# Kernel optimization log

Measured on AMD Instinct MI355X. Metric: run time of the kernel, lower is better.

Reference implementation:

```python
import jax, jax.numpy as jnp
import numpy as np

KS = 2
K = 3 * KS**2 + 3 * KS + 1  # 19 hex-stencil sites
MUL = 16                     # multiplicity of each irrep block
C0 = 0.28209479177387814     # Y_0 integral-normalized, 1/(2*sqrt(pi))
C1 = 0.4886025119029199      # Y_1 coeff, sqrt(3/(4*pi))


def _hex_offsets(ks):
    """Hexagonal stencil offsets in the exact order of spin2coltri2d (center first)."""
    hexagon = [[1, 1], [1, 0], [0, -1], [-1, -1], [-1, 0], [0, 1]]
    offs = [(0, 0)]
    for k in range(1, ks + 1):
        for l in range(6 * k):
            eb = hexagon[l // k]
            ea = hexagon[(l // k + 1) % 6]
            offs.append((eb[0] * (k - l % k) + ea[0] * (l % k),
                         eb[1] * (k - l % k) + ea[1] * (l % k)))
    return offs  # length K


def setup_inputs() -> dict:
    key = jax.random.key(0)
    k1, k2, k3, k4, k5, k6, k7 = jax.random.split(key, 7)
    N, Lx, Ly = 4, 128, 128
    feat = jax.random.normal(k1, (N, Lx, Ly, 4 * MUL), dtype=jnp.float32)
    spin = jax.random.normal(k2, (N, Lx, Ly, 3), dtype=jnp.float32)
    # 'uvw' TensorProduct weights: one (mul_in, mul_out) block per hex position per path
    wshape = (K, MUL, MUL)
    w000 = jax.random.normal(k3, wshape, dtype=jnp.float32)  # 0e x 0e -> 0e
    w011 = jax.random.normal(k4, wshape, dtype=jnp.float32)  # 0e x 1e -> 1e
    w101 = jax.random.normal(k5, wshape, dtype=jnp.float32)  # 1e x 0e -> 1e
    w110 = jax.random.normal(k6, wshape, dtype=jnp.float32)  # 1e x 1e -> 0e (dot)
    w111 = jax.random.normal(k7, wshape, dtype=jnp.float32)  # 1e x 1e -> 1e (cross)
    return {"feat": feat, "spin": spin, "w000": w000, "w011": w011,
            "w101": w101, "w110": w110, "w111": w111}


def reference(feat, spin, w000, w011, w101, w110, w111):
    # --- spin2coltri2d: circular hex-stencil gather via rolls (no pad copy) ---
    offs = _hex_offsets(KS)
    col = jnp.stack([jnp.roll(feat, shift=(-ox, -oy), axis=(1, 2))
                     for (ox, oy) in offs], axis=3)  # (N,Lx,Ly,K,64)
    s = col[..., :MUL]                                       # scalars (N,Lx,Ly,K,16)
    v = col[..., MUL:].reshape(col.shape[:4] + (MUL, 3))     # vectors (N,Lx,Ly,K,16,3)
    # --- spherical harmonics of spin, l=0..1, normalize=False, integral norm ---
    sh1 = C1 * spin[..., jnp.array([1, 2, 0])]               # e3nn l=1 order (y,z,x)
    # --- CG tensor product, path-normalized per output irrep ---
    a_s = 1.0 / np.sqrt(2 * K * MUL)   # two paths feed scalar out
    a_v = 1.0 / np.sqrt(3 * K * MUL)   # three paths feed vector out
    out_s = C0 * jnp.einsum('nxyku,kuw->nxyw', s, w000)
    out_s = out_s + jnp.einsum('nxykui,nxyi,kuw->nxyw', v, sh1, w110) / np.sqrt(3.0)
    out_s = a_s * out_s
    out_v = jnp.einsum('nxyku,nxyi,kuw->nxywi', s, sh1, w011)
    out_v = out_v + C0 * jnp.einsum('nxykui,kuw->nxywi', v, w101)
    cross = jnp.cross(v, sh1[:, :, :, None, None, :])        # 1e x 1e -> 1e
    out_v = out_v + jnp.einsum('nxykui,kuw->nxywi', cross, w111) / np.sqrt(2.0)
    out_v = a_v * out_v
    return jnp.concatenate(
        [out_s, out_v.reshape(out_v.shape[:3] + (3 * MUL,))], axis=-1)
```

## Files before the change

kernel.cpp:

```cpp
#include <hip/hip_runtime.h>

typedef __attribute__((ext_vector_type(8))) short short8;
typedef __attribute__((ext_vector_type(4))) float f32x4;

#define C0F 0.28209479177387814f
#define C1F 0.4886025119029199f
#define IS3 0.5773502691896258f
#define IS2 0.7071067811865476f
#define ASC 0.040555354f
#define AVC 0.033113308f

#define FEAT_STRIDE 144
#define W_LDS_BASE 20736
#define W_M_STRIDE 10240
#define LDS_TOTAL (20736 + 5 * 10240)

__constant__ int c_doff[20] = {0, 13, 12, -1, -13, -12, 1,
                               26, 25, 24, 11, -2, -14, -26, -25, -24, -11, 2, 14, 0};

__device__ inline unsigned short f32_bf16(float x) {
    unsigned int u = __float_as_uint(x);
    return (unsigned short)((u + 0x7FFF + ((u >> 16) & 1)) >> 16);
}

__global__ __launch_bounds__(256) void wprep_kernel(
    const float* __restrict__ w000, const float* __restrict__ w011,
    const float* __restrict__ w101, const float* __restrict__ w110,
    const float* __restrict__ w111, unsigned short* __restrict__ wout)
{
    int o = blockIdx.x * 256 + threadIdx.x;
    int m = o / 5120;
    int r1 = o - m * 5120;
    int tap = r1 >> 8;
    int r2 = r1 & 255;
    int w = r2 >> 4;
    int u = r2 & 15;
    const float* W = (m == 0) ? w000 : (m == 1) ? w011 : (m == 2) ? w101 : (m == 3) ? w110 : w111;
    float val = (tap < 19) ? W[tap * 256 + u * 16 + w] : 0.0f;
    wout[o] = f32_bf16(val);
}

__global__ __launch_bounds__(256) void spinconv_mfma(
    const float* __restrict__ feat, const float* __restrict__ spin,
    const unsigned short* __restrict__ wbf, float* __restrict__ out)
{
    extern __shared__ char smem[];
    const int tid = threadIdx.x;
    const int b = blockIdx.x;
    const int n = b >> 8;
    const int X0 = ((b >> 4) & 15) << 3;
    const int Y0 = (b & 15) << 3;

    for (int r = 0; r < 13; ++r) {
        int off = r * 4096 + tid * 16;
        if (off < 51200) {
            short8 v = *(const short8*)((const char*)wbf + off);
            *(short8*)(smem + W_LDS_BASE + off) = v;
        }
    }
    for (int r = 0; r < 9; ++r) {
        int p = (tid >> 4) + (r << 4);
        int j4 = tid & 15;
        int dx = p / 12, dy = p - dx * 12;
        int gx = (X0 - 2 + dx) & 127;
        int gy = (Y0 - 2 + dy) & 127;
        const float4 v = ((const float4*)(feat + ((((n << 7) + gx) << 7) + gy) * 64))[j4];
        char* dstb = smem + p * FEAT_STRIDE;
        float vals[4] = {v.x, v.y, v.z, v.w};
        int ch0 = j4 * 4;
#pragma unroll
        for (int c = 0; c < 4; ++c) {
            int ch = ch0 + c;
            int j = ch - 16;
            int dst = (ch < 16) ? ch : (16 + 16 * (j % 3) + j / 3);
            *(unsigned short*)(dstb + dst * 2) = f32_bf16(vals[c]);
        }
    }
    __syncthreads();

    const int lane = tid & 63;
    const int wave = tid >> 6;
    const int lx = lane & 15;
    const int q = lane >> 4;
    const int u0b = (q & 1) << 4;
    const int taph = q >> 1;
    const int ploc = (wave << 4) + lx;
    const int slot0 = ((ploc >> 3) + 2) * 12 + ((ploc & 7) + 2);
    const char* wlds = smem + W_LDS_BASE;

    f32x4 aS0{0,0,0,0}, aS1{0,0,0,0};
    f32x4 aB0{0,0,0,0}, aB1{0,0,0,0}, aB2{0,0,0,0};
    f32x4 aC0{0,0,0,0}, aC1{0,0,0,0}, aC2{0,0,0,0};
    f32x4 aD0{0,0,0,0}, aD1{0,0,0,0}, aD2{0,0,0,0};

#pragma unroll
    for (int t = 0; t < 10; ++t) {
        const int tap = 2 * t + taph;
        const char* ab = smem + (slot0 + c_doff[tap]) * FEAT_STRIDE + u0b;
        short8 a_s  = *(const short8*)(ab);
        short8 a_v0 = *(const short8*)(ab + 32);
        short8 a_v1 = *(const short8*)(ab + 64);
        short8 a_v2 = *(const short8*)(ab + 96);
        const char* bb = wlds + tap * 512 + lx * 32 + u0b;
        short8 b000 = *(const short8*)(bb);
        short8 b011 = *(const short8*)(bb + 1 * W_M_STRIDE);
        short8 b101 = *(const short8*)(bb + 2 * W_M_STRIDE);
        short8 b110 = *(const short8*)(bb + 3 * W_M_STRIDE);
        short8 b111 = *(const short8*)(bb + 4 * W_M_STRIDE);
        aS0 = __builtin_amdgcn_mfma_f32_16x16x32_bf16(a_s,  b000, aS0, 0, 0, 0);
        aS1 = __builtin_amdgcn_mfma_f32_16x16x32_bf16(a_s,  b011, aS1, 0, 0, 0);
        aB0 = __builtin_amdgcn_mfma_f32_16x16x32_bf16(a_v0, b101, aB0, 0, 0, 0);
        aC0 = __builtin_amdgcn_mfma_f32_16x16x32_bf16(a_v0, b110, aC0, 0, 0, 0);
        aD0 = __builtin_amdgcn_mfma_f32_16x16x32_bf16(a_v0, b111, aD0, 0, 0, 0);
        aB1 = __builtin_amdgcn_mfma_f32_16x16x32_bf16(a_v1, b101, aB1, 0, 0, 0);
        aC1 = __builtin_amdgcn_mfma_f32_16x16x32_bf16(a_v1, b110, aC1, 0, 0, 0);
        aD1 = __builtin_amdgcn_mfma_f32_16x16x32_bf16(a_v1, b111, aD1, 0, 0, 0);
        aB2 = __builtin_amdgcn_mfma_f32_16x16x32_bf16(a_v2, b101, aB2, 0, 0, 0);
        aC2 = __builtin_amdgcn_mfma_f32_16x16x32_bf16(a_v2, b110, aC2, 0, 0, 0);
        aD2 = __builtin_amdgcn_mfma_f32_16x16x32_bf16(a_v2, b111, aD2, 0, 0, 0);
    }

    const int w = lx;
#pragma unroll
    for (int r = 0; r < 4; ++r) {
        const int pl = (wave << 4) + (q << 2) + r;
        const int gx = X0 + (pl >> 3);
        const int gy = Y0 + (pl & 7);
        const int P = (((n << 7) + gx) << 7) + gy;
        const float s0 = C1F * spin[3 * P + 1];
        const float s1 = C1F * spin[3 * P + 2];
        const float s2 = C1F * spin[3 * P + 0];
        float* o = out + (size_t)P * 64;
        o[w] = ASC * (C0F * aS0[r] + IS3 * (s0 * aC0[r] + s1 * aC1[r] + s2 * aC2[r]));
        o[16 + 3 * w + 0] = AVC * (s0 * aS1[r] + C0F * aB0[r] + IS2 * (s2 * aD1[r] - s1 * aD2[r]));
        o[16 + 3 * w + 1] = AVC * (s1 * aS1[r] + C0F * aB1[r] + IS2 * (s0 * aD2[r] - s2 * aD0[r]));
        o[16 + 3 * w + 2] = AVC * (s2 * aS1[r] + C0F * aB2[r] + IS2 * (s1 * aD0[r] - s0 * aD1[r]));
    }
}

extern "C" void kernel_launch(void* const* d_in, const int* in_sizes, int n_in,
                              void* d_out, int out_size, void* d_ws, size_t ws_size,
                              hipStream_t stream) {
    const float* feat = (const float*)d_in[0];
    const float* spin = (const float*)d_in[1];
    const float* w000 = (const float*)d_in[2];
    const float* w011 = (const float*)d_in[3];
    const float* w101 = (const float*)d_in[4];
    const float* w110 = (const float*)d_in[5];
    const float* w111 = (const float*)d_in[6];
    float* out = (float*)d_out;
    unsigned short* wbf = (unsigned short*)d_ws;

    static bool attr_set = false;
    if (!attr_set) {
        (void)hipFuncSetAttribute((const void*)spinconv_mfma,
                                  hipFuncAttributeMaxDynamicSharedMemorySize, LDS_TOTAL);
        attr_set = true;
    }

    hipLaunchKernelGGL(wprep_kernel, dim3(100), dim3(256), 0, stream,
                       w000, w011, w101, w110, w111, wbf);
    hipLaunchKernelGGL(spinconv_mfma, dim3(1024), dim3(256), LDS_TOTAL, stream,
                       feat, spin, wbf, out);
}
```

Measured before the change: 95.48 us.

## Pre-convert features to swizzled bf16 and load tiles via global_load_lds

The prep kernel now also converts the whole feature tensor to bf16 in the permuted scalar/vector channel layout, writing 128-byte rows with an XOR swizzle keyed on position. The main kernel then stages weights and the haloed feature tile straight into LDS with async global_load_lds, with no per-thread conversion or scatter stores, and reads features with the matching swizzle to avoid bank conflicts. Spin values are also loaded before the staging so their latency overlaps. This trades an extra full pass over the features plus a bf16 workspace round trip for a cheaper, conflict-free staging phase in the main kernel.

```diff
diff --git a/kernel.cpp b/kernel.cpp
--- a/kernel.cpp
+++ b/kernel.cpp
@@ -2,6 +2,7 @@
 
 typedef __attribute__((ext_vector_type(8))) short short8;
 typedef __attribute__((ext_vector_type(4))) float f32x4;
+typedef __attribute__((ext_vector_type(4))) int i32x4;
 
 #define C0F 0.28209479177387814f
 #define C1F 0.4886025119029199f
@@ -10,10 +11,9 @@
 #define ASC 0.040555354f
 #define AVC 0.033113308f
 
-#define FEAT_STRIDE 144
-#define W_LDS_BASE 20736
-#define W_M_STRIDE 10240
-#define LDS_TOTAL (20736 + 5 * 10240)
+#define WBYTES 51200
+#define FLDS   51200
+#define LDS_TOTAL (51200 + 18432)
 
 __constant__ int c_doff[20] = {0, 13, 12, -1, -13, -12, 1,
                                26, 25, 24, 11, -2, -14, -26, -25, -24, -11, 2, 14, 0};
@@ -23,70 +23,105 @@
     return (unsigned short)((u + 0x7FFF + ((u >> 16) & 1)) >> 16);
 }
 
-__global__ __launch_bounds__(256) void wprep_kernel(
+#define GLD16(gp, lp) __builtin_amdgcn_global_load_lds( \
+    (const __attribute__((address_space(1))) unsigned int*)(gp), \
+    (__attribute__((address_space(3))) unsigned int*)(lp), 16, 0, 0)
+
+__global__ __launch_bounds__(256) void prep_kernel(
+    const float* __restrict__ feat,
     const float* __restrict__ w000, const float* __restrict__ w011,
     const float* __restrict__ w101, const float* __restrict__ w110,
-    const float* __restrict__ w111, unsigned short* __restrict__ wout)
+    const float* __restrict__ w111, unsigned char* __restrict__ ws)
 {
-    int o = blockIdx.x * 256 + threadIdx.x;
-    int m = o / 5120;
-    int r1 = o - m * 5120;
-    int tap = r1 >> 8;
-    int r2 = r1 & 255;
-    int w = r2 >> 4;
-    int u = r2 & 15;
-    const float* W = (m == 0) ? w000 : (m == 1) ? w011 : (m == 2) ? w101 : (m == 3) ? w110 : w111;
-    float val = (tap < 19) ? W[tap * 256 + u * 16 + w] : 0.0f;
-    wout[o] = f32_bf16(val);
+    const int t = threadIdx.x;
+    if (blockIdx.x >= 2048) {
+        int o = (blockIdx.x - 2048) * 256 + t;
+        int m = o / 5120;
+        int r1 = o - m * 5120;
+        int tap = r1 >> 8;
+        int r2 = r1 & 255;
+        int w = r2 >> 4;
+        int u = r2 & 15;
+        const float* W = (m == 0) ? w000 : (m == 1) ? w011 : (m == 2) ? w101 : (m == 3) ? w110 : w111;
+        float val = (tap < 19) ? W[tap * 256 + u * 16 + w] : 0.0f;
+        ((unsigned short*)ws)[o] = f32_bf16(val);
+        return;
+    }
+    __shared__ float raw[2048];
+    const int P0 = blockIdx.x * 32;
+    const float4* src = (const float4*)feat + (size_t)P0 * 16;
+    float4 l0 = src[t * 2];
+    float4 l1 = src[t * 2 + 1];
+    *(float4*)&raw[t * 8] = l0;
+    *(float4*)&raw[t * 8 + 4] = l1;
+    __syncthreads();
+    const int p = t >> 3;
+    const int c = t & 7;
+    const float* r = &raw[p * 64];
+    int ch0, stride;
+    if (c < 2) { ch0 = c * 8; stride = 1; }
+    else { int i = (c - 2) >> 1, uh = (c - 2) & 1; ch0 = 16 + i + 24 * uh; stride = 3; }
+    unsigned int pk[4];
+#pragma unroll
+    for (int e = 0; e < 4; ++e) {
+        unsigned int lo = f32_bf16(r[ch0 + stride * (2 * e)]);
+        unsigned int hi = f32_bf16(r[ch0 + stride * (2 * e + 1)]);
+        pk[e] = lo | (hi << 16);
+    }
+    const int PX = P0 + p;
+    const int gy = PX & 127, gx = (PX >> 7) & 127;
+    const int k = (4 * gx + gy + 2) & 7;
+    *(i32x4*)(ws + WBYTES + (size_t)PX * 128 + ((c ^ k) << 4)) = *(const i32x4*)pk;
 }
 
 __global__ __launch_bounds__(256) void spinconv_mfma(
-    const float* __restrict__ feat, const float* __restrict__ spin,
-    const unsigned short* __restrict__ wbf, float* __restrict__ out)
+    const unsigned char* __restrict__ ws, const float* __restrict__ spin,
+    float* __restrict__ out)
 {
     extern __shared__ char smem[];
-    const int tid = threadIdx.x;
-    const int b = blockIdx.x;
+    const int tid = threadIdx.x, b = blockIdx.x;
     const int n = b >> 8;
     const int X0 = ((b >> 4) & 15) << 3;
     const int Y0 = (b & 15) << 3;
-
-    for (int r = 0; r < 13; ++r) {
-        int off = r * 4096 + tid * 16;
-        if (off < 51200) {
-            short8 v = *(const short8*)((const char*)wbf + off);
-            *(short8*)(smem + W_LDS_BASE + off) = v;
-        }
-    }
-    for (int r = 0; r < 9; ++r) {
-        int p = (tid >> 4) + (r << 4);
-        int j4 = tid & 15;
-        int dx = p / 12, dy = p - dx * 12;
-        int gx = (X0 - 2 + dx) & 127;
-        int gy = (Y0 - 2 + dy) & 127;
-        const float4 v = ((const float4*)(feat + ((((n << 7) + gx) << 7) + gy) * 64))[j4];
-        char* dstb = smem + p * FEAT_STRIDE;
-        float vals[4] = {v.x, v.y, v.z, v.w};
-        int ch0 = j4 * 4;
-#pragma unroll
-        for (int c = 0; c < 4; ++c) {
-            int ch = ch0 + c;
-            int j = ch - 16;
-            int dst = (ch < 16) ? ch : (16 + 16 * (j % 3) + j / 3);
-            *(unsigned short*)(dstb + dst * 2) = f32_bf16(vals[c]);
-        }
-    }
-    __syncthreads();
-
-    const int lane = tid & 63;
-    const int wave = tid >> 6;
+    const int lane = tid & 63, wv = tid >> 6;
     const int lx = lane & 15;
     const int q = lane >> 4;
+
+    float sp[12];
+#pragma unroll
+    for (int r = 0; r < 4; ++r) {
+        const int pl = (wv << 4) + (q << 2) + r;
+        const int P = ((((n << 7) + X0 + (pl >> 3)) << 7) + Y0 + (pl & 7));
+        sp[r * 3 + 0] = spin[3 * P + 0];
+        sp[r * 3 + 1] = spin[3 * P + 1];
+        sp[r * 3 + 2] = spin[3 * P + 2];
+    }
+
+    for (int j = 0; j < 13; ++j) {
+        const int cid = j * 4 + wv;
+        if (cid < 50)
+            GLD16(ws + cid * 1024 + lane * 16, smem + cid * 1024);
+    }
+    const unsigned char* fsrc = ws + WBYTES;
+    for (int j = 0; j < 5; ++j) {
+        const int cid = wv + 4 * j;
+        if (cid < 18) {
+            const int px = cid * 8 + (lane >> 3);
+            const int cc = lane & 7;
+            const int dx = px / 12, dy = px - dx * 12;
+            const int gx = (X0 - 2 + dx) & 127;
+            const int gy = (Y0 - 2 + dy) & 127;
+            GLD16(fsrc + (size_t)((((n << 7) + gx) << 7) + gy) * 128 + cc * 16,
+                  smem + FLDS + cid * 1024);
+        }
+    }
+    __syncthreads();
+
     const int u0b = (q & 1) << 4;
     const int taph = q >> 1;
-    const int ploc = (wave << 4) + lx;
+    const int ploc = (wv << 4) + lx;
     const int slot0 = ((ploc >> 3) + 2) * 12 + ((ploc & 7) + 2);
-    const char* wlds = smem + W_LDS_BASE;
+    const char* flds = smem + FLDS;
 
     f32x4 aS0{0,0,0,0}, aS1{0,0,0,0};
     f32x4 aB0{0,0,0,0}, aB1{0,0,0,0}, aB2{0,0,0,0};
@@ -96,17 +131,19 @@
 #pragma unroll
     for (int t = 0; t < 10; ++t) {
         const int tap = 2 * t + taph;
-        const char* ab = smem + (slot0 + c_doff[tap]) * FEAT_STRIDE + u0b;
-        short8 a_s  = *(const short8*)(ab);
-        short8 a_v0 = *(const short8*)(ab + 32);
-        short8 a_v1 = *(const short8*)(ab + 64);
-        short8 a_v2 = *(const short8*)(ab + 96);
-        const char* bb = wlds + tap * 512 + lx * 32 + u0b;
+        const int st = slot0 + c_doff[tap];
+        const char* ab = flds + st * 128;
+        const int key = (st & 7) << 4;
+        short8 a_s  = *(const short8*)(ab + ((u0b      ) ^ key));
+        short8 a_v0 = *(const short8*)(ab + ((u0b + 32) ^ key));
+        short8 a_v1 = *(const short8*)(ab + ((u0b + 64) ^ key));
+        short8 a_v2 = *(const short8*)(ab + ((u0b + 96) ^ key));
+        const char* bb = smem + tap * 512 + lx * 32 + u0b;
         short8 b000 = *(const short8*)(bb);
-        short8 b011 = *(const short8*)(bb + 1 * W_M_STRIDE);
-        short8 b101 = *(const short8*)(bb + 2 * W_M_STRIDE);
-        short8 b110 = *(const short8*)(bb + 3 * W_M_STRIDE);
-        short8 b111 = *(const short8*)(bb + 4 * W_M_STRIDE);
+        short8 b011 = *(const short8*)(bb + 1 * 10240);
+        short8 b101 = *(const short8*)(bb + 2 * 10240);
+        short8 b110 = *(const short8*)(bb + 3 * 10240);
+        short8 b111 = *(const short8*)(bb + 4 * 10240);
         aS0 = __builtin_amdgcn_mfma_f32_16x16x32_bf16(a_s,  b000, aS0, 0, 0, 0);
         aS1 = __builtin_amdgcn_mfma_f32_16x16x32_bf16(a_s,  b011, aS1, 0, 0, 0);
         aB0 = __builtin_amdgcn_mfma_f32_16x16x32_bf16(a_v0, b101, aB0, 0, 0, 0);
@@ -123,13 +160,13 @@
     const int w = lx;
 #pragma unroll
     for (int r = 0; r < 4; ++r) {
-        const int pl = (wave << 4) + (q << 2) + r;
+        const int pl = (wv << 4) + (q << 2) + r;
         const int gx = X0 + (pl >> 3);
         const int gy = Y0 + (pl & 7);
         const int P = (((n << 7) + gx) << 7) + gy;
-        const float s0 = C1F * spin[3 * P + 1];
-        const float s1 = C1F * spin[3 * P + 2];
-        const float s2 = C1F * spin[3 * P + 0];
+        const float s0 = C1F * sp[r * 3 + 1];
+        const float s1 = C1F * sp[r * 3 + 2];
+        const float s2 = C1F * sp[r * 3 + 0];
         float* o = out + (size_t)P * 64;
         o[w] = ASC * (C0F * aS0[r] + IS3 * (s0 * aC0[r] + s1 * aC1[r] + s2 * aC2[r]));
         o[16 + 3 * w + 0] = AVC * (s0 * aS1[r] + C0F * aB0[r] + IS2 * (s2 * aD1[r] - s1 * aD2[r]));
@@ -149,7 +186,7 @@
     const float* w110 = (const float*)d_in[5];
     const float* w111 = (const float*)d_in[6];
     float* out = (float*)d_out;
-    unsigned short* wbf = (unsigned short*)d_ws;
+    unsigned char* ws = (unsigned char*)d_ws;
 
     static bool attr_set = false;
     if (!attr_set) {
@@ -158,8 +195,8 @@
         attr_set = true;
     }
 
-    hipLaunchKernelGGL(wprep_kernel, dim3(100), dim3(256), 0, stream,
-                       w000, w011, w101, w110, w111, wbf);
+    hipLaunchKernelGGL(prep_kernel, dim3(2148), dim3(256), 0, stream,
+                       feat, w000, w011, w101, w110, w111, ws);
     hipLaunchKernelGGL(spinconv_mfma, dim3(1024), dim3(256), LDS_TOTAL, stream,
-                       feat, spin, wbf, out);
-}
+                       ws, spin, out);
+}
```

New measurement: 92.46 us. 3.2% less time.
